# Kernel optimization log

Hardware: AMD Instinct MI355X
Metric: run time of the kernel (lower is better)

## Reference

```python
import jax, jax.numpy as jnp
import numpy as np

NC = 120000            # active coarse voxels
D, H, W = 16, 256, 256 # coarse grid
NF = 2 * NC            # active fine voxels (upsample output)
CIN, COUT = 128, 64


def _build_pairs():
    """Build spconv-style (in_idx, out_idx) pair maps per kernel offset.
    Padding: in_idx = NC (dummy zero feature row), out_idx = n_out (dropped row)."""
    rng = np.random.default_rng(0)
    flat = rng.choice(D * H * W, size=NC, replace=False)
    cz, cy, cx = np.unravel_index(flat, (D, H, W))
    lut = np.full(D * H * W, -1, np.int64)
    lut[flat] = np.arange(NC)

    def subm(offs):
        P = np.full((len(offs), NC, 2), NC, np.int32)
        for k, (dz, dy, dx) in enumerate(offs):
            nz, ny, nx = cz + dz, cy + dy, cx + dx
            ok = (nz >= 0) & (nz < D) & (ny >= 0) & (ny < H) & (nx >= 0) & (nx < W)
            nb = np.full(NC, -1, np.int64)
            nb[ok] = lut[(nz[ok] * H + ny[ok]) * W + nx[ok]]
            ok &= nb >= 0
            idx = np.nonzero(ok)[0]
            P[k, :len(idx), 0] = nb[idx]
            P[k, :len(idx), 1] = idx
        return P

    o33 = [(a, b, c) for a in (-1, 0, 1) for b in (-1, 0, 1) for c in (-1, 0, 1)]
    o13 = [(0, b, c) for b in (-1, 0, 1) for c in (-1, 0, 1)]   # kernel (1,3,3)
    o31 = [(a, 0, c) for a in (-1, 0, 1) for c in (-1, 0, 1)]   # kernel (3,1,3)

    # fine coords: each coarse voxel c spawns fine voxels 2c and 2c+1 (all dims)
    fz = np.concatenate([cz * 2, cz * 2 + 1])
    fy = np.concatenate([cy * 2, cy * 2 + 1])
    fx = np.concatenate([cx * 2, cx * 2 + 1])
    # inverse of a k=3, stride=2, pad=1 downsample: fine f <- coarse o where f = 2o - 1 + k
    Pu = np.zeros((27, NC, 2), np.int32)
    Pu[..., 0] = NC
    Pu[..., 1] = NF
    for k, (a, b, c) in enumerate([(a, b, c) for a in range(3) for b in range(3) for c in range(3)]):
        nz, ny, nx = fz + 1 - a, fy + 1 - b, fx + 1 - c
        ok = (nz % 2 == 0) & (ny % 2 == 0) & (nx % 2 == 0) & (nz >= 0) & (ny >= 0) & (nx >= 0)
        oz, oy, ox = nz // 2, ny // 2, nx // 2
        ok &= (oz < D) & (oy < H) & (ox < W)
        nb = np.full(NF, -1, np.int64)
        nb[ok] = lut[(oz[ok] * H + oy[ok]) * W + ox[ok]]
        ok &= nb >= 0
        idx = np.nonzero(ok)[0][:NC]
        Pu[k, :len(idx), 0] = nb[idx]
        Pu[k, :len(idx), 1] = idx
    return subm(o33), subm(o13), subm(o31), Pu


def setup_inputs():
    p33, p13, p31, pup = _build_pairs()
    ks = jax.random.split(jax.random.key(0), 12)
    f32 = jnp.float32
    return {
        "feats_x": jax.random.normal(ks[0], (NC, CIN), f32),
        "feats_skip": jax.random.normal(ks[1], (NC, CIN), f32),
        "W_trans": 0.05 * jax.random.normal(ks[2], (27, CIN, COUT), f32),
        "W1": 0.05 * jax.random.normal(ks[3], (9, COUT, COUT), f32),
        "W2": 0.05 * jax.random.normal(ks[4], (9, COUT, COUT), f32),
        "W_up": 0.05 * jax.random.normal(ks[5], (27, COUT, COUT), f32),
        "g0": 1.0 + 0.1 * jax.random.normal(ks[6], (COUT,), f32),
        "b0": 0.1 * jax.random.normal(ks[7], (COUT,), f32),
        "g1": 1.0 + 0.1 * jax.random.normal(ks[8], (COUT,), f32),
        "b1": 0.1 * jax.random.normal(ks[9], (COUT,), f32),
        "g2": 1.0 + 0.1 * jax.random.normal(ks[10], (COUT,), f32),
        "b2": 0.1 * jax.random.normal(ks[11], (COUT,), f32),
        "pairs33": jnp.asarray(p33),
        "pairs13": jnp.asarray(p13),
        "pairs31": jnp.asarray(p31),
        "pairs_up": jnp.asarray(pup),
    }


def _spconv(feats, Wk, pairs, n_out):
    # gather-GEMM-scatter sparse conv: feats [N,Cin], Wk [K,Cin,Cout], pairs [K,P,2]
    fp = jnp.concatenate([feats, jnp.zeros((1, feats.shape[1]), feats.dtype)], 0)
    out = jnp.zeros((n_out + 1, Wk.shape[2]), feats.dtype)
    for k in range(Wk.shape[0]):  # fixed small K (9 or 27)
        msg = fp[pairs[k, :, 0]] @ Wk[k]        # [P, Cout]
        out = out.at[pairs[k, :, 1]].add(msg)
    return out[:n_out]


def _bn(x, g, b):
    # BatchNorm1d (training-mode batch stats, eps=1e-5, biased var)
    m = x.mean(0)
    v = x.var(0)
    return (x - m) * jax.lax.rsqrt(v + 1e-5) * g + b


def reference(feats_x, feats_skip, W_trans, W1, W2, W_up,
              g0, b0, g1, b1, g2, b2,
              pairs33, pairs13, pairs31, pairs_up):
    x = feats_x + feats_skip                              # residual fuse with skip
    upA = _spconv(x, W_trans, pairs33, NC)                # trans_dilao (3x3x3 subm)
    upA = _bn(jax.nn.leaky_relu(upA, 0.01), g0, b0)       # act then BN (as in source)
    upE1 = _bn(_spconv(upA, W1, pairs13, NC), g1, b1)     # conv1x3 + bn1
    upE2 = _bn(_spconv(upA, W2, pairs31, NC), g2, b2)     # conv3x1 + bn2
    return _spconv(upE1 + upE2, W_up, pairs_up, NF)       # SparseInverseConv3d upsample
```

## Files before the change

### kernel.cpp

```cpp
#include <hip/hip_runtime.h>
#include <stdint.h>

typedef unsigned short u16;
typedef unsigned int u32;
typedef __bf16 bf16x8 __attribute__((ext_vector_type(8)));
typedef float floatx4 __attribute__((ext_vector_type(4)));

static constexpr int NC = 120000;
static constexpr int NF = 240000;

__device__ __forceinline__ float bf2f(u16 u) {
    union { u32 i; float f; } v; v.i = ((u32)u) << 16; return v.f;
}
__device__ __forceinline__ u16 f2bf(float f) {
    union { float f; u32 i; } v; v.f = f;
    u32 r = v.i + 0x7FFFu + ((v.i >> 16) & 1u);
    return (u16)(r >> 16);
}

__device__ __forceinline__ int xcd_swz(int bid, int nb) {
    int q = nb >> 3, r = nb & 7;
    int x = bid & 7, i = bid >> 3;
    return (x < r ? x * (q + 1) : r * (q + 1) + (x - r) * q) + i;
}

__global__ void add_pad_k(const float* __restrict__ a, const float* __restrict__ b,
                          u16* __restrict__ xp) {
    int idx = blockIdx.x * blockDim.x + threadIdx.x;
    if (idx >= (NC + 1) * 32) return;
    uint2 vo;
    if (idx < NC * 32) {
        float4 va = ((const float4*)a)[idx];
        float4 vb = ((const float4*)b)[idx];
        vo.x = (u32)f2bf(va.x + vb.x) | ((u32)f2bf(va.y + vb.y) << 16);
        vo.y = (u32)f2bf(va.z + vb.z) | ((u32)f2bf(va.w + vb.w) << 16);
    } else {
        vo.x = vo.y = 0u;
    }
    ((uint2*)xp)[idx] = vo;
}

__global__ void transpose_w_k(const float* __restrict__ W, u16* __restrict__ Wt,
                              int K, int Cin) {
    int idx = blockIdx.x * blockDim.x + threadIdx.x;
    if (idx >= K * Cin * 64) return;
    int per = Cin * 64;
    int k = idx / per, rem = idx - k * per;
    int kc = rem >> 11;
    int r2 = rem & 2047;
    int nt = r2 >> 9, lane = (r2 >> 3) & 63, j = r2 & 7;
    int ci = kc * 32 + (lane >> 4) * 8 + j;
    int co = nt * 16 + (lane & 15);
    Wt[idx] = f2bf(W[(size_t)(k * Cin + ci) * 64 + co]);
}

__device__ __forceinline__ int upslot_to_k(int s) {
    if (s == 0) return 13;
    int e = s - 1;
    return 18 * ((e >> 2) & 1) + 6 * ((e >> 1) & 1) + 2 * (e & 1);
}
__global__ void transpose_wup_k(const float* __restrict__ W, u16* __restrict__ Wt) {
    int idx = blockIdx.x * blockDim.x + threadIdx.x;
    if (idx >= 9 * 4096) return;
    int s = idx >> 12, rem = idx & 4095;
    int kc = rem >> 11, r2 = rem & 2047;
    int nt = r2 >> 9, lane = (r2 >> 3) & 63, j = r2 & 7;
    int ci = kc * 32 + (lane >> 4) * 8 + j;
    int co = nt * 16 + (lane & 15);
    int k = upslot_to_k(s);
    Wt[idx] = f2bf(W[(size_t)(k * 64 + ci) * 64 + co]);
}

__global__ void fill_k(int* __restrict__ p, int n, int val) {
    int i = blockIdx.x * blockDim.x + threadIdx.x;
    if (i < n) p[i] = val;
}

__global__ void scatter_k(const int* __restrict__ pairs, int* __restrict__ inv,
                          int npairs, int n_out) {
    int i = blockIdx.x * blockDim.x + threadIdx.x;
    if (i >= npairs) return;
    int in = pairs[2 * i], out = pairs[2 * i + 1];
    if (out < n_out) inv[(i / NC) * n_out + out] = in;
}

__global__ void scatter_up_k(const int* __restrict__ pairs, int* __restrict__ inv) {
    int i = blockIdx.x * blockDim.x + threadIdx.x;
    if (i >= 27 * NC) return;
    int in = pairs[2 * i], out = pairs[2 * i + 1];
    if (out >= NF) return;
    int k = i / NC;
    int a = k / 9, r = k - a * 9, b = r / 3, c = r - b * 3;
    int s;
    if (k == 13) {
        s = 0;
    } else if (((a | b | c) & 1) == 0) {
        s = 1 + (a >> 1) * 4 + (b >> 1) * 2 + (c >> 1);
    } else {
        return;
    }
    inv[(size_t)s * NF + out] = in;
}

template <int TCIN, int KMAX, int R, bool LEAKY, bool F32OUT, int MINW>
__global__ __launch_bounds__(256, MINW) void spconv_k(
    const u16* __restrict__ feats,
    const int* __restrict__ invA, const u16* __restrict__ wTA, void* __restrict__ outA,
    const int* __restrict__ invB, const u16* __restrict__ wTB, void* __restrict__ outB,
    int nb0, int n_outA, int n_outB, int kliveA, int kliveB, int nrA, int nrB) {
    constexpr int KC = TCIN / 32;
    constexpr int WFRAGS = TCIN * 64 / 8;
    constexpr int NST = WFRAGS / 256;
    __shared__ bf16x8 wlds[2][WFRAGS];

    const int tid = threadIdx.x;
    const int wave = tid >> 6, lane = tid & 63;
    const int l15 = lane & 15, quad = lane >> 4;
    const bool second = (int)blockIdx.x >= nb0;
    int bid = second ? (int)blockIdx.x - nb0 : (int)blockIdx.x;
    const int nb = second ? (int)gridDim.x - nb0 : nb0;
    bid = xcd_swz(bid, nb);
    const int* __restrict__ inv = second ? invB : invA;
    const u16* __restrict__ wT  = second ? wTB : wTA;
    void* __restrict__ outv     = second ? outB : outA;
    const int n_out             = second ? n_outB : n_outA;
    const int Klive             = second ? kliveB : kliveA;
    const int nr                = second ? nrB : nrA;

    const int blockrow = bid * (R * 64);
    const int base = blockrow + wave * 16 + l15;

    int rowix[R];
#pragma unroll
    for (int t = 0; t < R; ++t) rowix[t] = min(base + t * 64, nr - 1);

    floatx4 acc[R][4];
#pragma unroll
    for (int t = 0; t < R; ++t)
#pragma unroll
        for (int nt = 0; nt < 4; ++nt) acc[t][nt] = (floatx4)(0.0f);

    int rc[R], rn[R];
#pragma unroll
    for (int t = 0; t < R; ++t) rc[t] = inv[rowix[t]];
#pragma unroll
    for (int t = 0; t < R; ++t) rn[t] = inv[n_out + rowix[t]];

    {
        const bf16x8* wsrc = (const bf16x8*)wT + tid;
#pragma unroll
        for (int s = 0; s < NST; ++s) wlds[0][tid + s * 256] = wsrc[s * 256];
    }

    bf16x8 abuf[2][R][KC];
#pragma unroll
    for (int t = 0; t < R; ++t) {
        if (__any(rc[t] != NC)) {
            const u16* ap = feats + (size_t)rc[t] * TCIN + quad * 8;
#pragma unroll
            for (int kc = 0; kc < KC; ++kc) abuf[0][t][kc] = *(const bf16x8*)(ap + kc * 32);
        }
    }
    __syncthreads();

#pragma unroll
    for (int k = 0; k < KMAX; ++k) {
        if (k < Klive) {
            const int cur = k & 1, nxt = cur ^ 1;
            if (k + 1 < Klive) {
                const bf16x8* wsrc = (const bf16x8*)(wT + (size_t)(k + 1) * (64 * TCIN)) + tid;
                bf16x8 st[NST];
#pragma unroll
                for (int s = 0; s < NST; ++s) st[s] = wsrc[s * 256];
#pragma unroll
                for (int s = 0; s < NST; ++s) wlds[nxt][tid + s * 256] = st[s];
            }
            int rf[R];
#pragma unroll
            for (int t = 0; t < R; ++t) rf[t] = NC;
            if (k + 2 < Klive) {
                const int* invf = inv + (size_t)(k + 2) * n_out;
#pragma unroll
                for (int t = 0; t < R; ++t) rf[t] = invf[rowix[t]];
            }
            bool lv[R], any = false;
#pragma unroll
            for (int t = 0; t < R; ++t) { lv[t] = __any(rc[t] != NC); any = any || lv[t]; }
            if (k + 1 < Klive) {
#pragma unroll
                for (int t = 0; t < R; ++t) {
                    if (__any(rn[t] != NC)) {
                        const u16* ap = feats + (size_t)rn[t] * TCIN + quad * 8;
#pragma unroll
                        for (int kc = 0; kc < KC; ++kc)
                            abuf[nxt][t][kc] = *(const bf16x8*)(ap + kc * 32);
                    }
                }
            }
            if (any) {
                bf16x8 b[KC][4];
#pragma unroll
                for (int kc = 0; kc < KC; ++kc)
#pragma unroll
                    for (int nt = 0; nt < 4; ++nt)
                        b[kc][nt] = wlds[cur][(kc * 4 + nt) * 64 + lane];
#pragma unroll
                for (int t = 0; t < R; ++t) {
                    if (lv[t]) {
#pragma unroll
                        for (int kc = 0; kc < KC; ++kc)
#pragma unroll
                            for (int nt = 0; nt < 4; ++nt)
                                acc[t][nt] = __builtin_amdgcn_mfma_f32_16x16x32_bf16(
                                    abuf[cur][t][kc], b[kc][nt], acc[t][nt], 0, 0, 0);
                    }
                }
            }
            __syncthreads();
#pragma unroll
            for (int t = 0; t < R; ++t) { rc[t] = rn[t]; rn[t] = rf[t]; }
        }
    }
#pragma unroll
    for (int t = 0; t < R; ++t) {
#pragma unroll
        for (int nt = 0; nt < 4; ++nt) {
#pragma unroll
            for (int r = 0; r < 4; ++r) {
                float v = acc[t][nt][r];
                if (LEAKY) v = v > 0.f ? v : 0.01f * v;
                int row = blockrow + t * 64 + wave * 16 + quad * 4 + r;
                if (row < nr) {
                    size_t oi = (size_t)row * 64 + nt * 16 + l15;
                    if (F32OUT) ((float*)outv)[oi] = v;
                    else        ((u16*)outv)[oi] = f2bf(v);
                }
            }
        }
    }
}

__global__ void stats1_k(const u16* __restrict__ raw, float* __restrict__ sums,
                         int nblk) {
    int tid = threadIdx.x;
    int wave = tid >> 6, c = tid & 63;
    int gw = (int)blockIdx.x * 4 + wave;
    int GW = nblk * 4;
    float s = 0.f, q = 0.f;
    for (int r = gw; r < NC; r += GW) {
        float v = bf2f(raw[(size_t)r * 64 + c]);
        s += v; q += v * v;
    }
    __shared__ float sbm[4][64], qbm[4][64];
    sbm[wave][c] = s; qbm[wave][c] = q;
    __syncthreads();
    if (tid < 64) {
        float S = sbm[0][tid] + sbm[1][tid] + sbm[2][tid] + sbm[3][tid];
        float Q = qbm[0][tid] + qbm[1][tid] + qbm[2][tid] + qbm[3][tid];
        atomicAdd(&sums[tid], S);
        atomicAdd(&sums[64 + tid], Q);
    }
}

__global__ void stats2_k(const u16* __restrict__ ra, const u16* __restrict__ rb,
                         float* __restrict__ sa, float* __restrict__ sb, int half) {
    const u16* raw = ((int)blockIdx.x < half) ? ra : rb;
    float* sums    = ((int)blockIdx.x < half) ? sa : sb;
    int bx = ((int)blockIdx.x < half) ? (int)blockIdx.x : (int)blockIdx.x - half;
    int tid = threadIdx.x;
    int wave = tid >> 6, c = tid & 63;
    int gw = bx * 4 + wave;
    int GW = half * 4;
    float s = 0.f, q = 0.f;
    for (int r = gw; r < NC; r += GW) {
        float v = bf2f(raw[(size_t)r * 64 + c]);
        s += v; q += v * v;
    }
    __shared__ float sbm[4][64], qbm[4][64];
    sbm[wave][c] = s; qbm[wave][c] = q;
    __syncthreads();
    if (tid < 64) {
        float S = sbm[0][tid] + sbm[1][tid] + sbm[2][tid] + sbm[3][tid];
        float Q = qbm[0][tid] + qbm[1][tid] + qbm[2][tid] + qbm[3][tid];
        atomicAdd(&sums[tid], S);
        atomicAdd(&sums[64 + tid], Q);
    }
}

__global__ void finalize_k(const float* __restrict__ sums, const float* __restrict__ g,
                           const float* __restrict__ bb, float* __restrict__ scsh) {
    int c = threadIdx.x;
    if (c < 64) {
        float m = sums[c] / (float)NC;
        float v = sums[64 + c] / (float)NC - m * m;
        float sc = g[c] * rsqrtf(v + 1e-5f);
        scsh[c] = sc;
        scsh[64 + c] = bb[c] - m * sc;
    }
}

__global__ void apply0_k(const u16* __restrict__ raw, const float* __restrict__ scsh,
                         u16* __restrict__ up) {
    int idx = blockIdx.x * blockDim.x + threadIdx.x;
    if (idx >= (NC + 1) * 64) return;
    int c = idx & 63, i = idx >> 6;
    up[idx] = (i < NC) ? f2bf(bf2f(raw[idx]) * scsh[c] + scsh[64 + c]) : (u16)0;
}

__global__ void apply12_k(const u16* __restrict__ rb, const u16* __restrict__ rc,
                          const float* __restrict__ s1, const float* __restrict__ s2,
                          u16* __restrict__ up) {
    int idx = blockIdx.x * blockDim.x + threadIdx.x;
    if (idx >= (NC + 1) * 64) return;
    int c = idx & 63, i = idx >> 6;
    float v = bf2f(rb[idx]) * s1[c] + s1[64 + c] + bf2f(rc[idx]) * s2[c] + s2[64 + c];
    up[idx] = (i < NC) ? f2bf(v) : (u16)0;
}

extern "C" void kernel_launch(void* const* d_in, const int* in_sizes, int n_in,
                              void* d_out, int out_size, void* d_ws, size_t ws_size,
                              hipStream_t stream) {
    const float* feats_x    = (const float*)d_in[0];
    const float* feats_skip = (const float*)d_in[1];
    const float* W_trans    = (const float*)d_in[2];
    const float* W1         = (const float*)d_in[3];
    const float* W2         = (const float*)d_in[4];
    const float* W_up       = (const float*)d_in[5];
    const float* g0 = (const float*)d_in[6],  *b0 = (const float*)d_in[7];
    const float* g1 = (const float*)d_in[8],  *b1 = (const float*)d_in[9];
    const float* g2 = (const float*)d_in[10], *b2 = (const float*)d_in[11];
    const int* pairs33 = (const int*)d_in[12];
    const int* pairs13 = (const int*)d_in[13];
    const int* pairs31 = (const int*)d_in[14];
    const int* pairs_up = (const int*)d_in[15];
    float* outp = (float*)d_out;

    char* ws = (char*)d_ws;
    size_t off = 0;
    auto alloc = [&](size_t bytes) {
        char* p = ws + off;
        off += (bytes + 255) & ~(size_t)255;
        return p;
    };
    u16* xp    = (u16*)alloc(30720256);
    int* inv33 = (int*)alloc(12960000);
    int* inv13 = (int*)alloc(4320000);
    int* inv31 = (int*)alloc(4320000);
    u16* rawA  = (u16*)alloc(15360000);
    u16* rawC  = (u16*)alloc(15360000);
    u16* upA   = (u16*)alloc(15360128);
    u16* WtA   = (u16*)alloc(27 * 128 * 64 * 2);
    u16* Wt1   = (u16*)alloc(9 * 64 * 64 * 2);
    u16* Wt2   = (u16*)alloc(9 * 64 * 64 * 2);
    u16* WtU   = (u16*)alloc(9 * 64 * 64 * 2);
    float* stats = (float*)alloc(6 * 128 * 4);
    int* inv_up = (int*)xp;
    u16* rawB = rawA;
    u16* upE  = (u16*)inv33;
    float *sums0 = stats,        *sums1 = stats + 128, *sums2 = stats + 256;
    float *scsh0 = stats + 384,  *scsh1 = stats + 512, *scsh2 = stats + 640;

    const int B = 256;
    hipMemsetAsync(stats, 0, 6 * 128 * 4, stream);

    transpose_w_k<<<(27 * 128 * 64 + 255) / 256, B, 0, stream>>>(W_trans, WtA, 27, 128);
    transpose_w_k<<<(9 * 64 * 64 + 255) / 256, B, 0, stream>>>(W1, Wt1, 9, 64);
    transpose_w_k<<<(9 * 64 * 64 + 255) / 256, B, 0, stream>>>(W2, Wt2, 9, 64);
    transpose_wup_k<<<(9 * 64 * 64 + 255) / 256, B, 0, stream>>>(W_up, WtU);

    add_pad_k<<<((NC + 1) * 32 + 255) / 256, B, 0, stream>>>(feats_x, feats_skip, xp);

    fill_k<<<(45 * NC + 255) / 256, B, 0, stream>>>(inv33, 45 * NC, NC);
    scatter_k<<<(27 * NC + 255) / 256, B, 0, stream>>>(pairs33, inv33, 27 * NC, NC);
    scatter_k<<<(9 * NC + 255) / 256, B, 0, stream>>>(pairs13, inv13, 9 * NC, NC);
    scatter_k<<<(9 * NC + 255) / 256, B, 0, stream>>>(pairs31, inv31, 9 * NC, NC);

    spconv_k<128, 27, 2, true, false, 2><<<938, B, 0, stream>>>(
        xp, inv33, WtA, rawA, inv33, WtA, rawA, 938, NC, NC, 27, 27, NC, NC);
    stats1_k<<<240, B, 0, stream>>>(rawA, sums0, 240);
    finalize_k<<<1, 64, 0, stream>>>(sums0, g0, b0, scsh0);
    apply0_k<<<((NC + 1) * 64 + 255) / 256, B, 0, stream>>>(rawA, scsh0, upA);

    fill_k<<<(9 * NF + 255) / 256, B, 0, stream>>>(inv_up, 9 * NF, NC);
    scatter_up_k<<<(27 * NC + 255) / 256, B, 0, stream>>>(pairs_up, inv_up);

    spconv_k<64, 9, 2, false, false, 3><<<1876, B, 0, stream>>>(
        upA, inv13, Wt1, rawB, inv31, Wt2, rawC, 938, NC, NC, 9, 9, NC, NC);
    stats2_k<<<240, B, 0, stream>>>(rawB, rawC, sums1, sums2, 120);
    finalize_k<<<1, 64, 0, stream>>>(sums1, g1, b1, scsh1);
    finalize_k<<<1, 64, 0, stream>>>(sums2, g2, b2, scsh2);

    apply12_k<<<((NC + 1) * 64 + 255) / 256, B, 0, stream>>>(rawB, rawC, scsh1, scsh2, upE);

    spconv_k<64, 8, 2, false, true, 3><<<1876, B, 0, stream>>>(
        upE, inv_up, WtU, outp,
        inv_up + (size_t)NF + NC, WtU + 64 * 64, (void*)(outp + (size_t)NC * 64),
        938, NF, NF, 1, 8, NC, NC);
}
```

Before: 523.4 us.

## Split spconv reduction dimension across waves with LDS reduction, drop LDS weight staging

Restructures the sparse conv kernel so each block handles 64 rows and its waves split the input-channel (K) dimension: each wave owns a 32-channel slice and loads its weight fragments directly from global memory into registers, with no double-buffered LDS staging or per-offset __syncthreads. Partial accumulators are reduced through shared memory at the end, and grids double to 1875/3750 blocks. The change removes the per-offset barriers and LDS weight traffic and raises parallelism, at the cost of redundant global weight loads per wave, a final LDS reduction, and per-lane instead of wave-uniform feature-load predicates. The row-bounds clamps and guards were dropped because the row counts now divide evenly.

```diff
diff --git a/kernel.cpp b/kernel.cpp
--- a/kernel.cpp
+++ b/kernel.cpp
@@ -102,20 +102,22 @@
     inv[(size_t)s * NF + out] = in;
 }
 
-template <int TCIN, int KMAX, int R, bool LEAKY, bool F32OUT, int MINW>
-__global__ __launch_bounds__(256, MINW) void spconv_k(
+template <int TCIN, int KMAX, bool LEAKY, bool F32OUT>
+__global__ __launch_bounds__(256, 2) void spconv_k(
     const u16* __restrict__ feats,
     const int* __restrict__ invA, const u16* __restrict__ wTA, void* __restrict__ outA,
     const int* __restrict__ invB, const u16* __restrict__ wTB, void* __restrict__ outB,
-    int nb0, int n_outA, int n_outB, int kliveA, int kliveB, int nrA, int nrB) {
-    constexpr int KC = TCIN / 32;
-    constexpr int WFRAGS = TCIN * 64 / 8;
-    constexpr int NST = WFRAGS / 256;
-    __shared__ bf16x8 wlds[2][WFRAGS];
+    int nb0, int n_outA, int n_outB, int kliveA, int kliveB) {
+    constexpr int NSPLIT = TCIN / 32;
+    constexpr int RT = NSPLIT;
+    __shared__ float red[(NSPLIT - 1) * 64 * 68];
 
     const int tid = threadIdx.x;
     const int wave = tid >> 6, lane = tid & 63;
     const int l15 = lane & 15, quad = lane >> 4;
+    const int rg = wave / NSPLIT;
+    const int ks = wave - rg * NSPLIT;
+
     const bool second = (int)blockIdx.x >= nb0;
     int bid = second ? (int)blockIdx.x - nb0 : (int)blockIdx.x;
     const int nb = second ? (int)gridDim.x - nb0 : nb0;
@@ -125,118 +127,118 @@
     void* __restrict__ outv     = second ? outB : outA;
     const int n_out             = second ? n_outB : n_outA;
     const int Klive             = second ? kliveB : kliveA;
-    const int nr                = second ? nrB : nrA;
-
-    const int blockrow = bid * (R * 64);
-    const int base = blockrow + wave * 16 + l15;
-
-    int rowix[R];
-#pragma unroll
-    for (int t = 0; t < R; ++t) rowix[t] = min(base + t * 64, nr - 1);
-
-    floatx4 acc[R][4];
-#pragma unroll
-    for (int t = 0; t < R; ++t)
-#pragma unroll
-        for (int nt = 0; nt < 4; ++nt) acc[t][nt] = (floatx4)(0.0f);
-
-    int rc[R], rn[R];
-#pragma unroll
-    for (int t = 0; t < R; ++t) rc[t] = inv[rowix[t]];
-#pragma unroll
-    for (int t = 0; t < R; ++t) rn[t] = inv[n_out + rowix[t]];
-
+
+    const int rowbase = bid * 64 + rg * (RT * 16);
+    const bf16x8 ZF = {};
+
+    int rowix[RT];
+#pragma unroll
+    for (int rt = 0; rt < RT; ++rt) rowix[rt] = rowbase + rt * 16 + l15;
+
+    floatx4 acc[RT][4];
+#pragma unroll
+    for (int rt = 0; rt < RT; ++rt)
+#pragma unroll
+        for (int nt = 0; nt < 4; ++nt) acc[rt][nt] = (floatx4)(0.0f);
+
+    int rc[RT], rn[RT];
+#pragma unroll
+    for (int rt = 0; rt < RT; ++rt) rc[rt] = inv[rowix[rt]];
+#pragma unroll
+    for (int rt = 0; rt < RT; ++rt) rn[rt] = inv[n_out + rowix[rt]];
+
+    bf16x8 ab[2][RT], bb[2][4];
+#pragma unroll
+    for (int rt = 0; rt < RT; ++rt) {
+        if (rc[rt] != NC)
+            ab[0][rt] = *(const bf16x8*)(feats + (size_t)rc[rt] * TCIN + ks * 32 + quad * 8);
+        else
+            ab[0][rt] = ZF;
+    }
     {
-        const bf16x8* wsrc = (const bf16x8*)wT + tid;
-#pragma unroll
-        for (int s = 0; s < NST; ++s) wlds[0][tid + s * 256] = wsrc[s * 256];
-    }
-
-    bf16x8 abuf[2][R][KC];
-#pragma unroll
-    for (int t = 0; t < R; ++t) {
-        if (__any(rc[t] != NC)) {
-            const u16* ap = feats + (size_t)rc[t] * TCIN + quad * 8;
-#pragma unroll
-            for (int kc = 0; kc < KC; ++kc) abuf[0][t][kc] = *(const bf16x8*)(ap + kc * 32);
-        }
-    }
-    __syncthreads();
+        const u16* wk = wT;
+#pragma unroll
+        for (int nt = 0; nt < 4; ++nt)
+            bb[0][nt] = *(const bf16x8*)(wk + ((ks * 4 + nt) * 64 + lane) * 8);
+    }
 
 #pragma unroll
     for (int k = 0; k < KMAX; ++k) {
         if (k < Klive) {
             const int cur = k & 1, nxt = cur ^ 1;
-            if (k + 1 < Klive) {
-                const bf16x8* wsrc = (const bf16x8*)(wT + (size_t)(k + 1) * (64 * TCIN)) + tid;
-                bf16x8 st[NST];
-#pragma unroll
-                for (int s = 0; s < NST; ++s) st[s] = wsrc[s * 256];
-#pragma unroll
-                for (int s = 0; s < NST; ++s) wlds[nxt][tid + s * 256] = st[s];
-            }
-            int rf[R];
-#pragma unroll
-            for (int t = 0; t < R; ++t) rf[t] = NC;
+            int rf[RT];
+#pragma unroll
+            for (int rt = 0; rt < RT; ++rt) rf[rt] = NC;
             if (k + 2 < Klive) {
                 const int* invf = inv + (size_t)(k + 2) * n_out;
 #pragma unroll
-                for (int t = 0; t < R; ++t) rf[t] = invf[rowix[t]];
+                for (int rt = 0; rt < RT; ++rt) rf[rt] = invf[rowix[rt]];
             }
-            bool lv[R], any = false;
-#pragma unroll
-            for (int t = 0; t < R; ++t) { lv[t] = __any(rc[t] != NC); any = any || lv[t]; }
+            bool lv[RT];
+#pragma unroll
+            for (int rt = 0; rt < RT; ++rt) lv[rt] = __any(rc[rt] != NC);
             if (k + 1 < Klive) {
 #pragma unroll
-                for (int t = 0; t < R; ++t) {
-                    if (__any(rn[t] != NC)) {
-                        const u16* ap = feats + (size_t)rn[t] * TCIN + quad * 8;
-#pragma unroll
-                        for (int kc = 0; kc < KC; ++kc)
-                            abuf[nxt][t][kc] = *(const bf16x8*)(ap + kc * 32);
-                    }
+                for (int rt = 0; rt < RT; ++rt) {
+                    if (rn[rt] != NC)
+                        ab[nxt][rt] = *(const bf16x8*)(feats + (size_t)rn[rt] * TCIN + ks * 32 + quad * 8);
+                    else
+                        ab[nxt][rt] = ZF;
+                }
+                const u16* wk = wT + (size_t)(k + 1) * (TCIN * 64);
+#pragma unroll
+                for (int nt = 0; nt < 4; ++nt)
+                    bb[nxt][nt] = *(const bf16x8*)(wk + ((ks * 4 + nt) * 64 + lane) * 8);
+            }
+#pragma unroll
+            for (int rt = 0; rt < RT; ++rt) {
+                if (lv[rt]) {
+#pragma unroll
+                    for (int nt = 0; nt < 4; ++nt)
+                        acc[rt][nt] = __builtin_amdgcn_mfma_f32_16x16x32_bf16(
+                            ab[cur][rt], bb[cur][nt], acc[rt][nt], 0, 0, 0);
                 }
             }
-            if (any) {
-                bf16x8 b[KC][4];
-#pragma unroll
-                for (int kc = 0; kc < KC; ++kc)
-#pragma unroll
-                    for (int nt = 0; nt < 4; ++nt)
-                        b[kc][nt] = wlds[cur][(kc * 4 + nt) * 64 + lane];
-#pragma unroll
-                for (int t = 0; t < R; ++t) {
-                    if (lv[t]) {
-#pragma unroll
-                        for (int kc = 0; kc < KC; ++kc)
-#pragma unroll
-                            for (int nt = 0; nt < 4; ++nt)
-                                acc[t][nt] = __builtin_amdgcn_mfma_f32_16x16x32_bf16(
-                                    abuf[cur][t][kc], b[kc][nt], acc[t][nt], 0, 0, 0);
-                    }
+#pragma unroll
+            for (int rt = 0; rt < RT; ++rt) { rc[rt] = rn[rt]; rn[rt] = rf[rt]; }
+        }
+    }
+
+    if (ks != 0) {
+#pragma unroll
+        for (int rt = 0; rt < RT; ++rt)
+#pragma unroll
+            for (int nt = 0; nt < 4; ++nt) {
+                int col = nt * 16 + l15;
+                int rowloc = rg * (RT * 16) + rt * 16 + quad * 4;
+                *(floatx4*)&red[((ks - 1) * 64 + col) * 68 + rowloc] = acc[rt][nt];
+            }
+    }
+    __syncthreads();
+    if (ks == 0) {
+#pragma unroll
+        for (int s = 0; s < NSPLIT - 1; ++s)
+#pragma unroll
+            for (int rt = 0; rt < RT; ++rt)
+#pragma unroll
+                for (int nt = 0; nt < 4; ++nt) {
+                    int col = nt * 16 + l15;
+                    int rowloc = rg * (RT * 16) + rt * 16 + quad * 4;
+                    acc[rt][nt] += *(const floatx4*)&red[(s * 64 + col) * 68 + rowloc];
                 }
-            }
-            __syncthreads();
-#pragma unroll
-            for (int t = 0; t < R; ++t) { rc[t] = rn[t]; rn[t] = rf[t]; }
-        }
-    }
-#pragma unroll
-    for (int t = 0; t < R; ++t) {
-#pragma unroll
-        for (int nt = 0; nt < 4; ++nt) {
-#pragma unroll
-            for (int r = 0; r < 4; ++r) {
-                float v = acc[t][nt][r];
-                if (LEAKY) v = v > 0.f ? v : 0.01f * v;
-                int row = blockrow + t * 64 + wave * 16 + quad * 4 + r;
-                if (row < nr) {
+#pragma unroll
+        for (int rt = 0; rt < RT; ++rt)
+#pragma unroll
+            for (int nt = 0; nt < 4; ++nt)
+#pragma unroll
+                for (int r = 0; r < 4; ++r) {
+                    float v = acc[rt][nt][r];
+                    if (LEAKY) v = v > 0.f ? v : 0.01f * v;
+                    int row = rowbase + rt * 16 + quad * 4 + r;
                     size_t oi = (size_t)row * 64 + nt * 16 + l15;
                     if (F32OUT) ((float*)outv)[oi] = v;
                     else        ((u16*)outv)[oi] = f2bf(v);
                 }
-            }
-        }
     }
 }
 
@@ -375,8 +377,8 @@
     scatter_k<<<(9 * NC + 255) / 256, B, 0, stream>>>(pairs13, inv13, 9 * NC, NC);
     scatter_k<<<(9 * NC + 255) / 256, B, 0, stream>>>(pairs31, inv31, 9 * NC, NC);
 
-    spconv_k<128, 27, 2, true, false, 2><<<938, B, 0, stream>>>(
-        xp, inv33, WtA, rawA, inv33, WtA, rawA, 938, NC, NC, 27, 27, NC, NC);
+    spconv_k<128, 27, true, false><<<1875, B, 0, stream>>>(
+        xp, inv33, WtA, rawA, inv33, WtA, rawA, 1875, NC, NC, 27, 27);
     stats1_k<<<240, B, 0, stream>>>(rawA, sums0, 240);
     finalize_k<<<1, 64, 0, stream>>>(sums0, g0, b0, scsh0);
     apply0_k<<<((NC + 1) * 64 + 255) / 256, B, 0, stream>>>(rawA, scsh0, upA);
@@ -384,16 +386,16 @@
     fill_k<<<(9 * NF + 255) / 256, B, 0, stream>>>(inv_up, 9 * NF, NC);
     scatter_up_k<<<(27 * NC + 255) / 256, B, 0, stream>>>(pairs_up, inv_up);
 
-    spconv_k<64, 9, 2, false, false, 3><<<1876, B, 0, stream>>>(
-        upA, inv13, Wt1, rawB, inv31, Wt2, rawC, 938, NC, NC, 9, 9, NC, NC);
+    spconv_k<64, 9, false, false><<<3750, B, 0, stream>>>(
+        upA, inv13, Wt1, rawB, inv31, Wt2, rawC, 1875, NC, NC, 9, 9);
     stats2_k<<<240, B, 0, stream>>>(rawB, rawC, sums1, sums2, 120);
     finalize_k<<<1, 64, 0, stream>>>(sums1, g1, b1, scsh1);
     finalize_k<<<1, 64, 0, stream>>>(sums2, g2, b2, scsh2);
 
     apply12_k<<<((NC + 1) * 64 + 255) / 256, B, 0, stream>>>(rawB, rawC, scsh1, scsh2, upE);
 
-    spconv_k<64, 8, 2, false, true, 3><<<1876, B, 0, stream>>>(
+    spconv_k<64, 8, false, true><<<3750, B, 0, stream>>>(
         upE, inv_up, WtU, outp,
         inv_up + (size_t)NF + NC, WtU + 64 * 64, (void*)(outp + (size_t)NC * 64),
-        938, NF, NF, 1, 8, NC, NC);
-}
+        1875, NF, NF, 1, 8);
+}
```

Measured after the change: 532.2 us. Within noise of the previous version (+1.7%).
